# Kernel optimization log

Measured on AMD Instinct MI355X. Metric: run time of the kernel, lower is better.

Reference implementation:

```python
import jax, jax.numpy as jnp
import numpy as np
from jax import lax

IN, H, L, NC = 1024, 256, 3, 8
B, T = 64, 512


def setup_inputs() -> dict:
    key = jax.random.key(0)
    ks = iter(jax.random.split(key, 32))
    def u(shape, fan_in):
        s = 1.0 / np.sqrt(fan_in)
        return jax.random.uniform(next(ks), shape, jnp.float32, -s, s)
    inp = {"x": jax.random.normal(next(ks), (B, T, IN), jnp.float32)}
    dims = [IN, H, H]
    for l in range(L):
        inp[f"Wih{l}"] = u((4 * H, dims[l]), H)
        inp[f"Whh{l}"] = u((4 * H, H), H)
        # combined bias b_ih + b_hh (mathematically identical)
        inp[f"b{l}"] = u((4 * H,), H) + u((4 * H,), H)
    inp["W1"] = u((128, H), H)
    inp["bfc1"] = u((128,), H)
    inp["W2"] = u((NC, 128), 128)
    inp["bfc2"] = u((NC,), 128)
    return inp


def _lstm_layer(x_tbd, Wih, Whh, b):
    # x_tbd: (T, B, D). Precompute input gates with one big GEMM.
    xg = jnp.einsum("tbd,gd->tbg", x_tbd, Wih) + b  # (T, B, 4H)
    h0 = jnp.zeros((x_tbd.shape[1], H), x_tbd.dtype)
    def step(carry, xg_t):
        h, c = carry
        g = xg_t + h @ Whh.T
        i, f, gg, o = jnp.split(g, 4, axis=-1)  # torch gate order i,f,g,o
        i, f, o = jax.nn.sigmoid(i), jax.nn.sigmoid(f), jax.nn.sigmoid(o)
        c = f * c + i * jnp.tanh(gg)
        h = o * jnp.tanh(c)
        return (h, c), h
    _, hs = lax.scan(step, (h0, h0), xg)
    return hs  # (T, B, H)


def reference(x, Wih0, Whh0, b0, Wih1, Whh1, b1, Wih2, Whh2, b2, W1, bfc1, W2, bfc2):
    h = jnp.transpose(x, (1, 0, 2))  # (T, B, IN)
    for Wih, Whh, b in ((Wih0, Whh0, b0), (Wih1, Whh1, b1), (Wih2, Whh2, b2)):
        h = _lstm_layer(h, Wih, Whh, b)
    last = h[-1]  # (B, H) output at final timestep
    z = jax.nn.relu(last @ W1.T + bfc1)
    return z @ W2.T + bfc2  # (B, NC)
```

## Files before the change

kernel.cpp:

```cpp
#include <hip/hip_runtime.h>
#include <hip/hip_cooperative_groups.h>
#include <cmath>

namespace cg = cooperative_groups;

#define IN_DIM 1024
#define HD 256
#define G4H 1024
#define BB 64
#define TT 512
#define NCLS 8

#define SLOT_STRIDE (HD * BB)
#define LAYER_STRIDE (4 * SLOT_STRIDE)

__device__ __forceinline__ float sigmoidf_(float x) {
    return 1.0f / (1.0f + __expf(-x));
}
__device__ __forceinline__ float tanhf_(float x) {
    return 2.0f / (1.0f + __expf(-2.0f * x)) - 1.0f;
}
__device__ __forceinline__ unsigned long long ld_agent_u64(const unsigned long long* p) {
    return __hip_atomic_load(p, __ATOMIC_RELAXED, __HIP_MEMORY_SCOPE_AGENT);
}
__device__ __forceinline__ void st_agent_u64(unsigned long long* p, unsigned long long v) {
    __hip_atomic_store(p, v, __ATOMIC_RELAXED, __HIP_MEMORY_SCOPE_AGENT);
}

#define GBM 128
#define GBN 128
#define GBK 16

__global__ __launch_bounds__(256) void xg0_gemm(const float* __restrict__ x,
                                                const float* __restrict__ Wih0,
                                                const float* __restrict__ b0,
                                                float* __restrict__ xg0T) {
    __shared__ float As[GBK][GBM];
    __shared__ float Bs[GBK][GBN];
    const int m0 = blockIdx.y * GBM;
    const int n0 = blockIdx.x * GBN;
    const int tid = threadIdx.x;
    const int tx = tid & 15;
    const int ty = tid >> 4;
    const int lr = tid >> 1;
    const int lk = (tid & 1) * 8;
    const int am = m0 + lr;
    const size_t arow = (size_t)(am & 63) * TT + (am >> 6);
    float acc[8][8] = {};
    for (int k0 = 0; k0 < IN_DIM; k0 += GBK) {
        const float4 a0 = *(const float4*)&x[arow * IN_DIM + k0 + lk];
        const float4 a1 = *(const float4*)&x[arow * IN_DIM + k0 + lk + 4];
        const float4 w0 = *(const float4*)&Wih0[(size_t)(n0 + lr) * IN_DIM + k0 + lk];
        const float4 w1 = *(const float4*)&Wih0[(size_t)(n0 + lr) * IN_DIM + k0 + lk + 4];
        __syncthreads();
        As[lk + 0][lr] = a0.x; As[lk + 1][lr] = a0.y; As[lk + 2][lr] = a0.z; As[lk + 3][lr] = a0.w;
        As[lk + 4][lr] = a1.x; As[lk + 5][lr] = a1.y; As[lk + 6][lr] = a1.z; As[lk + 7][lr] = a1.w;
        Bs[lk + 0][lr] = w0.x; Bs[lk + 1][lr] = w0.y; Bs[lk + 2][lr] = w0.z; Bs[lk + 3][lr] = w0.w;
        Bs[lk + 4][lr] = w1.x; Bs[lk + 5][lr] = w1.y; Bs[lk + 6][lr] = w1.z; Bs[lk + 7][lr] = w1.w;
        __syncthreads();
#pragma unroll
        for (int k = 0; k < GBK; ++k) {
            const float4 av0 = *(const float4*)&As[k][ty * 8];
            const float4 av1 = *(const float4*)&As[k][ty * 8 + 4];
            const float4 bv0 = *(const float4*)&Bs[k][tx * 8];
            const float4 bv1 = *(const float4*)&Bs[k][tx * 8 + 4];
            const float am8[8] = {av0.x, av0.y, av0.z, av0.w, av1.x, av1.y, av1.z, av1.w};
            const float bn8[8] = {bv0.x, bv0.y, bv0.z, bv0.w, bv1.x, bv1.y, bv1.z, bv1.w};
#pragma unroll
            for (int i = 0; i < 8; ++i)
#pragma unroll
                for (int jj = 0; jj < 8; ++jj)
                    acc[i][jj] = fmaf(am8[i], bn8[jj], acc[i][jj]);
        }
    }
    const float4 bias0 = *(const float4*)&b0[n0 + tx * 8];
    const float4 bias1 = *(const float4*)&b0[n0 + tx * 8 + 4];
    const float bia[8] = {bias0.x, bias0.y, bias0.z, bias0.w, bias1.x, bias1.y, bias1.z, bias1.w};
#pragma unroll
    for (int i = 0; i < 8; ++i) {
        const int m = m0 + ty * 8 + i;
        const int t = m >> 6;
        const int bb = m & 63;
#pragma unroll
        for (int jj = 0; jj < 8; ++jj) {
            const int n = n0 + tx * 8 + jj;
            xg0T[((size_t)t * G4H + n) * BB + bb] = acc[i][jj] + bia[jj];
        }
    }
}

__global__ __launch_bounds__(512) void lstm_cells(
    const float* __restrict__ xg0T,
    const float* __restrict__ Whh0,
    const float* __restrict__ Wih1, const float* __restrict__ Whh1, const float* __restrict__ b1,
    const float* __restrict__ Wih2, const float* __restrict__ Whh2, const float* __restrict__ b2,
    unsigned long long* __restrict__ ringU, int* __restrict__ flags)
{
    cg::grid_group grid = cg::this_grid();
    const int blk = blockIdx.x;
    const int layer = blk >> 6;
    const int lb = blk & 63;
    const int jbase = lb * 4;
    const int tid = threadIdx.x;
    const int w = tid >> 6;
    const int b = tid & 63;
    const int kbase = w * 32;

    __shared__ float red[16][8][64];

    const float* Wih = (layer == 1) ? Wih1 : Wih2;
    const float* Whh = (layer == 0) ? Whh0 : ((layer == 1) ? Whh1 : Whh2);
    const float* bias = (layer == 1) ? b1 : b2;

    float whreg[8];
    float wihreg[8];
    {
        const int r = b >> 2;
        const int jl = r >> 2;
        const int g = r & 3;
        const int kofs = kbase + (b & 3) * 8;
        const float4 h0 = *(const float4*)&Whh[(size_t)(g * HD + jbase + jl) * HD + kofs];
        const float4 h1 = *(const float4*)&Whh[(size_t)(g * HD + jbase + jl) * HD + kofs + 4];
        whreg[0] = h0.x; whreg[1] = h0.y; whreg[2] = h0.z; whreg[3] = h0.w;
        whreg[4] = h1.x; whreg[5] = h1.y; whreg[6] = h1.z; whreg[7] = h1.w;
        if (layer > 0) {
            const float4 i0 = *(const float4*)&Wih[(size_t)(g * HD + jbase + jl) * HD + kofs];
            const float4 i1 = *(const float4*)&Wih[(size_t)(g * HD + jbase + jl) * HD + kofs + 4];
            wihreg[0] = i0.x; wihreg[1] = i0.y; wihreg[2] = i0.z; wihreg[3] = i0.w;
            wihreg[4] = i1.x; wihreg[5] = i1.y; wihreg[6] = i1.z; wihreg[7] = i1.w;
        } else {
#pragma unroll
            for (int u = 0; u < 8; ++u) wihreg[u] = 0.0f;
        }
    }

    for (int i = blk * 512 + tid; i < 3 * LAYER_STRIDE; i += 192 * 512) ringU[i] = 0ull;
    for (int i = blk * 512 + tid; i < 3 * TT * 64; i += 192 * 512) flags[i] = 0;

    float bs0 = 0.f, bs1 = 0.f, bs2 = 0.f, bs3 = 0.f;
    if (layer > 0 && tid < 256) {
        bs0 = bias[0 * HD + jbase + w]; bs1 = bias[1 * HD + jbase + w];
        bs2 = bias[2 * HD + jbase + w]; bs3 = bias[3 * HD + jbase + w];
    }

    unsigned long long* myU = ringU + (size_t)layer * LAYER_STRIDE;
    const unsigned long long* inU = ringU + (size_t)(layer - 1) * LAYER_STRIDE;

    float c = 0.0f;

    grid.sync();

    for (int t = 0; t < TT; ++t) {
        float xv0, xv1, xv2, xv3;
        if (layer == 0 && tid < 256) {
            const float* xg = xg0T + ((size_t)t * G4H + jbase + w) * BB + b;
            xv0 = xg[0 * HD * BB]; xv1 = xg[1 * HD * BB];
            xv2 = xg[2 * HD * BB]; xv3 = xg[3 * HD * BB];
        }
        __atomic_signal_fence(__ATOMIC_SEQ_CST);

        if (layer < 2 && t >= 4 && tid < 64) {
            const int* f_nxt = &flags[((layer + 1) * TT + (t - 4)) * 64 + tid];
            for (;;) {
                int ok = __hip_atomic_load(f_nxt, __ATOMIC_RELAXED, __HIP_MEMORY_SCOPE_AGENT);
                if (__all(ok)) break;
                __builtin_amdgcn_s_sleep(2);
            }
        }

        float hv[32];
        {
            const unsigned long long* hp = myU + (size_t)((t + 3) & 3) * SLOT_STRIDE
                                         + (size_t)kbase * BB + b;
            const unsigned want = (unsigned)t;
            unsigned long long v[32];
            for (;;) {
#pragma unroll
                for (int u = 0; u < 32; ++u) v[u] = ld_agent_u64(hp + (size_t)u * BB);
                unsigned ok = 1;
#pragma unroll
                for (int u = 0; u < 32; ++u) ok &= ((unsigned)(v[u] >> 32) == want) ? 1u : 0u;
                if (__all(ok != 0)) break;
                __builtin_amdgcn_s_sleep(2);
            }
#pragma unroll
            for (int u = 0; u < 32; ++u) hv[u] = __uint_as_float((unsigned)v[u]);
        }

        float gv[32];
        if (layer > 0) {
            const unsigned long long* gp = inU + (size_t)(t & 3) * SLOT_STRIDE
                                         + (size_t)kbase * BB + b;
            const unsigned want = (unsigned)(t + 1);
            unsigned long long v[32];
            for (;;) {
#pragma unroll
                for (int u = 0; u < 32; ++u) v[u] = ld_agent_u64(gp + (size_t)u * BB);
                unsigned ok = 1;
#pragma unroll
                for (int u = 0; u < 32; ++u) ok &= ((unsigned)(v[u] >> 32) == want) ? 1u : 0u;
                if (__all(ok != 0)) break;
                __builtin_amdgcn_s_sleep(2);
            }
#pragma unroll
            for (int u = 0; u < 32; ++u) gv[u] = __uint_as_float((unsigned)v[u]);
        }

        float acc[16];
#pragma unroll
        for (int r = 0; r < 16; ++r) {
            float a = 0.0f;
#pragma unroll
            for (int q = 0; q < 4; ++q) {
#pragma unroll
                for (int u = 0; u < 8; ++u) {
                    const float ws = __uint_as_float(
                        __builtin_amdgcn_readlane(__float_as_uint(whreg[u]), r * 4 + q));
                    a = fmaf(ws, hv[q * 8 + u], a);
                }
            }
            acc[r] = a;
        }
        if (layer > 0) {
#pragma unroll
            for (int r = 0; r < 16; ++r) {
                float a = acc[r];
#pragma unroll
                for (int q = 0; q < 4; ++q) {
#pragma unroll
                    for (int u = 0; u < 8; ++u) {
                        const float ws = __uint_as_float(
                            __builtin_amdgcn_readlane(__float_as_uint(wihreg[u]), r * 4 + q));
                        a = fmaf(ws, gv[q * 8 + u], a);
                    }
                }
                acc[r] = a;
            }
        }

#pragma unroll
        for (int r = 0; r < 16; ++r) red[r][w][b] = acc[r];
        __syncthreads();

        if (tid == 0) {
            __hip_atomic_store(&flags[(layer * TT + t) * 64 + lb], 1,
                               __ATOMIC_RELAXED, __HIP_MEMORY_SCOPE_AGENT);
        }

        if (tid < 256) {
            float a0, a1, a2, a3;
            if (layer == 0) { a0 = xv0; a1 = xv1; a2 = xv2; a3 = xv3; }
            else            { a0 = bs0; a1 = bs1; a2 = bs2; a3 = bs3; }
#pragma unroll
            for (int ww = 0; ww < 8; ++ww) {
                a0 += red[w * 4 + 0][ww][b];
                a1 += red[w * 4 + 1][ww][b];
                a2 += red[w * 4 + 2][ww][b];
                a3 += red[w * 4 + 3][ww][b];
            }
            const float ig = sigmoidf_(a0);
            const float fg = sigmoidf_(a1);
            const float gg = tanhf_(a2);
            const float og = sigmoidf_(a3);
            c = fg * c + ig * gg;
            const float h = og * tanhf_(c);
            const unsigned long long pk =
                ((unsigned long long)(unsigned)(t + 1) << 32) |
                (unsigned long long)__float_as_uint(h);
            st_agent_u64(&myU[(size_t)(t & 3) * SLOT_STRIDE
                              + (size_t)(jbase + w) * BB + b], pk);
        }

        __syncthreads();
    }
}

__global__ __launch_bounds__(256) void classifier_k(
    const unsigned long long* __restrict__ ringU,
    const float* __restrict__ W1, const float* __restrict__ bfc1,
    const float* __restrict__ W2, const float* __restrict__ bfc2,
    float* __restrict__ out)
{
    __shared__ float z[BB * 128];
    const unsigned long long* h2T = ringU + 2 * LAYER_STRIDE
                                  + (size_t)((TT - 1) & 3) * SLOT_STRIDE;
    const int tid = threadIdx.x;
    for (int idx = tid; idx < BB * 128; idx += 256) {
        const int bb = idx >> 7;
        const int n = idx & 127;
        float acc = bfc1[n];
        const float* wr = W1 + (size_t)n * HD;
        for (int k = 0; k < HD; ++k) {
            const float hval = __uint_as_float((unsigned)h2T[(size_t)k * BB + bb]);
            acc = fmaf(hval, wr[k], acc);
        }
        z[bb * 128 + n] = fmaxf(acc, 0.0f);
    }
    __syncthreads();
    for (int idx = tid; idx < BB * NCLS; idx += 256) {
        const int bb = idx >> 3;
        const int n = idx & 7;
        float acc = bfc2[n];
        const float* zr = &z[bb * 128];
        const float* wr = W2 + (size_t)n * 128;
        for (int k = 0; k < 128; k += 4) {
            const float4 zv = *(const float4*)&zr[k];
            const float4 wv = *(const float4*)&wr[k];
            acc = fmaf(zv.x, wv.x, acc); acc = fmaf(zv.y, wv.y, acc);
            acc = fmaf(zv.z, wv.z, acc); acc = fmaf(zv.w, wv.w, acc);
        }
        out[idx] = acc;
    }
}

extern "C" void kernel_launch(void* const* d_in, const int* in_sizes, int n_in,
                              void* d_out, int out_size, void* d_ws, size_t ws_size,
                              hipStream_t stream) {
    const float* x    = (const float*)d_in[0];
    const float* Wih0 = (const float*)d_in[1];
    const float* Whh0 = (const float*)d_in[2];
    const float* b0   = (const float*)d_in[3];
    const float* Wih1 = (const float*)d_in[4];
    const float* Whh1 = (const float*)d_in[5];
    const float* b1   = (const float*)d_in[6];
    const float* Wih2 = (const float*)d_in[7];
    const float* Whh2 = (const float*)d_in[8];
    const float* b2   = (const float*)d_in[9];
    const float* W1   = (const float*)d_in[10];
    const float* bfc1 = (const float*)d_in[11];
    const float* W2   = (const float*)d_in[12];
    const float* bfc2 = (const float*)d_in[13];

    float* xg0T = (float*)d_ws;
    unsigned long long* ringU =
        (unsigned long long*)(xg0T + (size_t)BB * TT * G4H);
    int* flags = (int*)(ringU + 3 * LAYER_STRIDE);

    xg0_gemm<<<dim3(G4H / GBN, (BB * TT) / GBM), 256, 0, stream>>>(x, Wih0, b0, xg0T);

    const float* xgc = xg0T;
    unsigned long long* ru = ringU;
    int* fl = flags;
    void* args[] = {
        (void*)&xgc, (void*)&Whh0,
        (void*)&Wih1, (void*)&Whh1, (void*)&b1,
        (void*)&Wih2, (void*)&Whh2, (void*)&b2,
        (void*)&ru, (void*)&fl
    };
    hipLaunchCooperativeKernel((void*)lstm_cells, dim3(192), dim3(512), args, 0, stream);

    classifier_k<<<1, 256, 0, stream>>>(ringU, W1, bfc1, W2, bfc2, (float*)d_out);
}
```

Before: 6.839 ms.

## Overlap input-gate matvec with recurrent-state wait and double-buffer reduction

The recurrent h loads are issued speculatively before the input-from-previous-layer path. The Wih·x contribution is computed first, while those loads are in flight, and only then does the code check the tag and spin on the recurrent state. The shared reduction buffer is double-buffered by timestep parity, which lets the trailing __syncthreads at the end of each step be removed. This shortens the serial critical path per step, at the cost of more registers live across the gv computation and twice the shared memory.

```diff
diff --git a/kernel.cpp b/kernel.cpp
--- a/kernel.cpp
+++ b/kernel.cpp
@@ -106,7 +106,7 @@
     const int b = tid & 63;
     const int kbase = w * 32;
 
-    __shared__ float red[16][8][64];
+    __shared__ float red[2][16][8][64];
 
     const float* Wih = (layer == 1) ? Wih1 : Wih2;
     const float* Whh = (layer == 0) ? Whh0 : ((layer == 1) ? Whh1 : Whh2);
@@ -151,6 +151,8 @@
     grid.sync();
 
     for (int t = 0; t < TT; ++t) {
+        const int p = t & 1;
+
         float xv0, xv1, xv2, xv3;
         if (layer == 0 && tid < 256) {
             const float* xg = xg0T + ((size_t)t * G4H + jbase + w) * BB + b;
@@ -168,63 +170,35 @@
             }
         }
 
-        float hv[32];
-        {
-            const unsigned long long* hp = myU + (size_t)((t + 3) & 3) * SLOT_STRIDE
-                                         + (size_t)kbase * BB + b;
-            const unsigned want = (unsigned)t;
-            unsigned long long v[32];
-            for (;;) {
-#pragma unroll
-                for (int u = 0; u < 32; ++u) v[u] = ld_agent_u64(hp + (size_t)u * BB);
-                unsigned ok = 1;
-#pragma unroll
-                for (int u = 0; u < 32; ++u) ok &= ((unsigned)(v[u] >> 32) == want) ? 1u : 0u;
-                if (__all(ok != 0)) break;
-                __builtin_amdgcn_s_sleep(2);
-            }
-#pragma unroll
-            for (int u = 0; u < 32; ++u) hv[u] = __uint_as_float((unsigned)v[u]);
-        }
-
-        float gv[32];
+        const unsigned long long* hp = myU + (size_t)((t + 3) & 3) * SLOT_STRIDE
+                                     + (size_t)kbase * BB + b;
+        unsigned long long v[32];
+#pragma unroll
+        for (int u = 0; u < 32; ++u) v[u] = ld_agent_u64(hp + (size_t)u * BB);
+        __atomic_signal_fence(__ATOMIC_SEQ_CST);
+
+        float acc[16];
+
         if (layer > 0) {
             const unsigned long long* gp = inU + (size_t)(t & 3) * SLOT_STRIDE
                                          + (size_t)kbase * BB + b;
-            const unsigned want = (unsigned)(t + 1);
-            unsigned long long v[32];
+            const unsigned wantg = (unsigned)(t + 1);
+            unsigned long long v2[32];
             for (;;) {
 #pragma unroll
-                for (int u = 0; u < 32; ++u) v[u] = ld_agent_u64(gp + (size_t)u * BB);
+                for (int u = 0; u < 32; ++u) v2[u] = ld_agent_u64(gp + (size_t)u * BB);
                 unsigned ok = 1;
 #pragma unroll
-                for (int u = 0; u < 32; ++u) ok &= ((unsigned)(v[u] >> 32) == want) ? 1u : 0u;
+                for (int u = 0; u < 32; ++u) ok &= ((unsigned)(v2[u] >> 32) == wantg) ? 1u : 0u;
                 if (__all(ok != 0)) break;
                 __builtin_amdgcn_s_sleep(2);
             }
-#pragma unroll
-            for (int u = 0; u < 32; ++u) gv[u] = __uint_as_float((unsigned)v[u]);
-        }
-
-        float acc[16];
-#pragma unroll
-        for (int r = 0; r < 16; ++r) {
-            float a = 0.0f;
-#pragma unroll
-            for (int q = 0; q < 4; ++q) {
-#pragma unroll
-                for (int u = 0; u < 8; ++u) {
-                    const float ws = __uint_as_float(
-                        __builtin_amdgcn_readlane(__float_as_uint(whreg[u]), r * 4 + q));
-                    a = fmaf(ws, hv[q * 8 + u], a);
-                }
-            }
-            acc[r] = a;
-        }
-        if (layer > 0) {
+            float gv[32];
+#pragma unroll
+            for (int u = 0; u < 32; ++u) gv[u] = __uint_as_float((unsigned)v2[u]);
 #pragma unroll
             for (int r = 0; r < 16; ++r) {
-                float a = acc[r];
+                float a = 0.0f;
 #pragma unroll
                 for (int q = 0; q < 4; ++q) {
 #pragma unroll
@@ -236,10 +210,45 @@
                 }
                 acc[r] = a;
             }
-        }
-
-#pragma unroll
-        for (int r = 0; r < 16; ++r) red[r][w][b] = acc[r];
+        } else {
+#pragma unroll
+            for (int r = 0; r < 16; ++r) acc[r] = 0.0f;
+        }
+
+        __atomic_signal_fence(__ATOMIC_SEQ_CST);
+
+        {
+            const unsigned want = (unsigned)t;
+            for (;;) {
+                unsigned ok = 1;
+#pragma unroll
+                for (int u = 0; u < 32; ++u) ok &= ((unsigned)(v[u] >> 32) == want) ? 1u : 0u;
+                if (__all(ok != 0)) break;
+                __builtin_amdgcn_s_sleep(2);
+#pragma unroll
+                for (int u = 0; u < 32; ++u) v[u] = ld_agent_u64(hp + (size_t)u * BB);
+            }
+        }
+        float hv[32];
+#pragma unroll
+        for (int u = 0; u < 32; ++u) hv[u] = __uint_as_float((unsigned)v[u]);
+#pragma unroll
+        for (int r = 0; r < 16; ++r) {
+            float a = acc[r];
+#pragma unroll
+            for (int q = 0; q < 4; ++q) {
+#pragma unroll
+                for (int u = 0; u < 8; ++u) {
+                    const float ws = __uint_as_float(
+                        __builtin_amdgcn_readlane(__float_as_uint(whreg[u]), r * 4 + q));
+                    a = fmaf(ws, hv[q * 8 + u], a);
+                }
+            }
+            acc[r] = a;
+        }
+
+#pragma unroll
+        for (int r = 0; r < 16; ++r) red[p][r][w][b] = acc[r];
         __syncthreads();
 
         if (tid == 0) {
@@ -253,10 +262,10 @@
             else            { a0 = bs0; a1 = bs1; a2 = bs2; a3 = bs3; }
 #pragma unroll
             for (int ww = 0; ww < 8; ++ww) {
-                a0 += red[w * 4 + 0][ww][b];
-                a1 += red[w * 4 + 1][ww][b];
-                a2 += red[w * 4 + 2][ww][b];
-                a3 += red[w * 4 + 3][ww][b];
+                a0 += red[p][w * 4 + 0][ww][b];
+                a1 += red[p][w * 4 + 1][ww][b];
+                a2 += red[p][w * 4 + 2][ww][b];
+                a3 += red[p][w * 4 + 3][ww][b];
             }
             const float ig = sigmoidf_(a0);
             const float fg = sigmoidf_(a1);
@@ -270,8 +279,6 @@
             st_agent_u64(&myU[(size_t)(t & 3) * SLOT_STRIDE
                               + (size_t)(jbase + w) * BB + b], pk);
         }
-
-        __syncthreads();
     }
 }
 
```

Result: slower. 7.099 ms (+3.8%).
